# Kernel tuning notes

Measured on AMD Instinct MI355X. Metric: run time of the kernel, lower is better.

The kernel has to match this reference:

```python
import jax, jax.numpy as jnp
import numpy as np

N, E, R, D_IN, D_H, D_OUT = 75000, 1200000, 8, 64, 64, 40


def setup_inputs() -> dict:
    key = jax.random.key(0)
    k_x, k_idx, k_rel, k_w1, k_w2 = jax.random.split(key, 5)
    x = jax.random.normal(k_x, (N, D_IN), dtype=jnp.float32)
    # Regular-degree CSR pointer: ptr[i+1]-ptr[i] = E//N = 16 (nondecreasing, ptr[0]=0, ptr[N]=E)
    ptr = jnp.arange(N + 1, dtype=jnp.int32) * (E // N)
    idx = jax.random.randint(k_idx, (E,), 0, N, dtype=jnp.int32)   # source node per edge
    rel = jax.random.randint(k_rel, (E,), 0, R, dtype=jnp.int32)   # relation type per edge
    W1 = jax.random.normal(k_w1, (R, D_IN, D_H), dtype=jnp.float32) / np.float32(np.sqrt(D_IN))
    W2 = jax.random.normal(k_w2, (R, D_H, D_OUT), dtype=jnp.float32) / np.float32(np.sqrt(D_H))
    return {"x": x, "ptr": ptr, "idx": idx, "rel": rel, "W1": W1, "W2": W2}


def _rgcn_conv(x, W, idx, rel, dst, num_node):
    # Typed transform for every (node, relation) pair: [N, R, F_out]
    xw = jnp.einsum('nd,rdf->nrf', x, W)
    # Per-edge gather of the relation-specific transformed source feature: [E, F_out]
    msg = xw[idx, rel]
    # Scatter-add into destination nodes (CSR rows)
    return jax.ops.segment_sum(msg, dst, num_segments=num_node)


def reference(x, ptr, idx, rel, W1, W2):
    num_edges = idx.shape[0]
    num_node = ptr.shape[0] - 1
    # CSR row id for each edge e: dst[e] = i s.t. ptr[i] <= e < ptr[i+1]
    dst = jnp.searchsorted(ptr, jnp.arange(num_edges, dtype=ptr.dtype), side='right') - 1
    h = _rgcn_conv(x, W1, idx, rel, dst, num_node)
    h = jax.nn.relu(h)  # dropout is identity in eval mode
    h = _rgcn_conv(h, W2, idx, rel, dst, num_node)
    return jax.nn.log_softmax(h, axis=-1)
```

## Files before the change

### kernel.cpp

```cpp
#include <hip/hip_runtime.h>
#include <hip/hip_bf16.h>


typedef __attribute__((ext_vector_type(8))) short short8;
typedef __attribute__((ext_vector_type(4))) float floatx4;

static __device__ __forceinline__ unsigned short f2bf(float f) {
    unsigned u = __float_as_uint(f);
    u += 0x7FFFu + ((u >> 16) & 1u);
    return (unsigned short)(u >> 16);
}
static __device__ __forceinline__ float bf2f(unsigned short h) {
    return __uint_as_float(((unsigned)h) << 16);
}

__global__ void k_cast(const float* __restrict__ x, unsigned short* __restrict__ o,
                       int n4, int np4) {
    int i = blockIdx.x * blockDim.x + threadIdx.x;
    if (i >= np4) return;
    ushort4 r;
    if (i < n4) {
        float4 v = ((const float4*)x)[i];
        r.x = f2bf(v.x); r.y = f2bf(v.y); r.z = f2bf(v.z); r.w = f2bf(v.w);
    } else {
        r.x = r.y = r.z = r.w = 0;
    }
    ((ushort4*)o)[i] = r;
}

__global__ void k_packw(const float* __restrict__ W1, const float* __restrict__ W2,
                        unsigned short* __restrict__ BT1, unsigned short* __restrict__ BT2) {
    int i = blockIdx.x * 256 + threadIdx.x;
    if (i < 512 * 64) {
        int j = i >> 6, d = i & 63;
        int r = j >> 6, f = j & 63;
        BT1[i] = f2bf(W1[r * 4096 + d * 64 + f]);
    } else if (i < 512 * 64 + 320 * 64) {
        int ii = i - 512 * 64;
        int j = ii >> 6, d = ii & 63;
        int r = j / 40, f = j - r * 40;
        BT2[ii] = f2bf(W2[r * 2560 + d * 40 + f]);
    }
}

__global__ __launch_bounds__(256) void k_xw(
    const unsigned short* __restrict__ A, const unsigned short* __restrict__ BT,
    unsigned short* __restrict__ xw, int NC, int nColBlk) {
    int bid = blockIdx.x;
    int cb = bid % nColBlk, rb = bid / nColBlk;
    int wave = threadIdx.x >> 6, lane = threadIdx.x & 63;
    int lr = lane & 15, lg = lane >> 4;
    int rowbase = rb * 256 + wave * 64;
    int col0 = cb * 64;
    floatx4 acc[4][4] = {};
#pragma unroll
    for (int k0 = 0; k0 < 2; ++k0) {
        int koff = k0 * 32 + lg * 8;
        short8 a[4], b[4];
#pragma unroll
        for (int mt = 0; mt < 4; ++mt)
            a[mt] = *(const short8*)(A + (size_t)(rowbase + mt * 16 + lr) * 64 + koff);
#pragma unroll
        for (int nt = 0; nt < 4; ++nt)
            b[nt] = *(const short8*)(BT + (size_t)(col0 + nt * 16 + lr) * 64 + koff);
#pragma unroll
        for (int mt = 0; mt < 4; ++mt)
#pragma unroll
            for (int nt = 0; nt < 4; ++nt)
                acc[mt][nt] = __builtin_amdgcn_mfma_f32_16x16x32_bf16(a[mt], b[nt], acc[mt][nt], 0, 0, 0);
    }
#pragma unroll
    for (int mt = 0; mt < 4; ++mt)
#pragma unroll
        for (int nt = 0; nt < 4; ++nt)
#pragma unroll
            for (int i = 0; i < 4; ++i) {
                int row = rowbase + mt * 16 + lg * 4 + i;
                xw[(size_t)row * NC + col0 + nt * 16 + lr] = f2bf(acc[mt][nt][i]);
            }
}

__global__ __launch_bounds__(256) void k_gs_relu(
    const unsigned short* __restrict__ xw,
    const int* __restrict__ ptr, const int* __restrict__ idx,
    const int* __restrict__ rel,
    unsigned short* __restrict__ H, int M, int MP) {
    int row = blockIdx.x * 4 + (threadIdx.x >> 6);
    int lane = threadIdx.x & 63;
    if (row >= MP) return;
    row = __builtin_amdgcn_readfirstlane(row);
    if (row >= M) { H[(size_t)row * 64 + lane] = 0; return; }
    int ps = ptr[row], pe = ptr[row + 1];
    int deg = pe - ps;
    const int* __restrict__ idxr = idx + ps;
    const int* __restrict__ relr = rel + ps;
    float c = 0.f;
    if (deg == 16) {
        float v[16];
#pragma unroll
        for (int t = 0; t < 16; ++t) {
            size_t o = ((size_t)idxr[t] * 8 + relr[t]) * 64;
            v[t] = bf2f(xw[o + lane]);
        }
#pragma unroll
        for (int t = 0; t < 16; ++t) c += v[t];
    } else {
        for (int t = 0; t < deg; ++t) {
            size_t o = ((size_t)idxr[t] * 8 + relr[t]) * 64;
            c += bf2f(xw[o + lane]);
        }
    }
    H[(size_t)row * 64 + lane] = f2bf(fmaxf(c, 0.f));
}

__global__ __launch_bounds__(256) void k_gs_lsm(
    const unsigned short* __restrict__ xw,
    const int* __restrict__ ptr, const int* __restrict__ idx,
    const int* __restrict__ rel,
    float* __restrict__ out, int M) {
    int row = blockIdx.x * 4 + (threadIdx.x >> 6);
    int lane = threadIdx.x & 63;
    if (row >= M) return;
    row = __builtin_amdgcn_readfirstlane(row);
    int ps = ptr[row], pe = ptr[row + 1];
    int deg = pe - ps;
    const int* __restrict__ idxr = idx + ps;
    const int* __restrict__ relr = rel + ps;
    bool ok = lane < 40;
    int l = ok ? lane : 0;
    float c = 0.f;
    if (deg == 16) {
        float v[16];
#pragma unroll
        for (int t = 0; t < 16; ++t) {
            size_t o = ((size_t)idxr[t] * 8 + relr[t]) * 40;
            v[t] = bf2f(xw[o + l]);
        }
#pragma unroll
        for (int t = 0; t < 16; ++t) c += v[t];
    } else {
        for (int t = 0; t < deg; ++t) {
            size_t o = ((size_t)idxr[t] * 8 + relr[t]) * 40;
            c += bf2f(xw[o + l]);
        }
    }
    float mx = ok ? c : -INFINITY;
#pragma unroll
    for (int m = 1; m < 64; m <<= 1) mx = fmaxf(mx, __shfl_xor(mx, m, 64));
    float e = ok ? __expf(c - mx) : 0.f;
    float s = e;
#pragma unroll
    for (int m = 1; m < 64; m <<= 1) s += __shfl_xor(s, m, 64);
    if (ok) out[(size_t)row * 40 + lane] = c - mx - __logf(s);
}

extern "C" void kernel_launch(void* const* d_in, const int* in_sizes, int n_in,
                              void* d_out, int out_size, void* d_ws, size_t ws_size,
                              hipStream_t stream) {
    const float* x  = (const float*)d_in[0];
    const int* ptr  = (const int*)d_in[1];
    const int* idx  = (const int*)d_in[2];
    const int* rel  = (const int*)d_in[3];
    const float* W1 = (const float*)d_in[4];
    const float* W2 = (const float*)d_in[5];
    float* out = (float*)d_out;

    int N = in_sizes[1] - 1;
    int MP = (N + 255) & ~255;

    char* ws = (char*)d_ws;
    size_t szRow64 = (size_t)MP * 64 * 2;
    unsigned short* xbf  = (unsigned short*)(ws);
    unsigned short* hbf  = (unsigned short*)(ws + szRow64);
    unsigned short* BT1  = (unsigned short*)(ws + 2 * szRow64);
    unsigned short* BT2  = (unsigned short*)(ws + 2 * szRow64 + 512 * 64 * 2);
    unsigned short* xwb  = (unsigned short*)(ws + 2 * szRow64 + 512 * 64 * 2 + 320 * 64 * 2);

    int n4 = N * 16, np4 = MP * 16;
    k_cast<<<(np4 + 255) / 256, 256, 0, stream>>>(x, xbf, n4, np4);
    k_packw<<<(512 * 64 + 320 * 64 + 255) / 256, 256, 0, stream>>>(W1, W2, BT1, BT2);

    int nrb = MP / 256;
    k_xw<<<nrb * 8, 256, 0, stream>>>(xbf, BT1, xwb, 512, 8);
    k_gs_relu<<<MP / 4, 256, 0, stream>>>(xwb, ptr, idx, rel, hbf, N, MP);
    k_xw<<<nrb * 5, 256, 0, stream>>>(hbf, BT2, xwb, 320, 5);
    k_gs_lsm<<<(N + 3) / 4, 256, 0, stream>>>(xwb, ptr, idx, rel, out, N);
}
```

Measured before the change: 129.8 us.

## Fuse fp32-to-bf16 cast into GEMM and gather two rows per wave

Removes the separate cast kernel by loading fp32 x directly in the first transform GEMM and converting to bf16 in registers, with row bounds checks. The two gather-sum kernels now process two destination rows per wavefront, each half-wave loading 4-byte bf16 pairs. This widens each lane's memory access and halves the wave count. The log-softmax reduction moves to 32-lane shuffles over paired features. This trades fewer launches and wider gathers for more index/address logic per wave, and each fp32 row is re-read by every column block of the first GEMM.

```diff
diff --git a/kernel.cpp b/kernel.cpp
--- a/kernel.cpp
+++ b/kernel.cpp
@@ -10,23 +10,8 @@
     u += 0x7FFFu + ((u >> 16) & 1u);
     return (unsigned short)(u >> 16);
 }
-static __device__ __forceinline__ float bf2f(unsigned short h) {
-    return __uint_as_float(((unsigned)h) << 16);
-}
-
-__global__ void k_cast(const float* __restrict__ x, unsigned short* __restrict__ o,
-                       int n4, int np4) {
-    int i = blockIdx.x * blockDim.x + threadIdx.x;
-    if (i >= np4) return;
-    ushort4 r;
-    if (i < n4) {
-        float4 v = ((const float4*)x)[i];
-        r.x = f2bf(v.x); r.y = f2bf(v.y); r.z = f2bf(v.z); r.w = f2bf(v.w);
-    } else {
-        r.x = r.y = r.z = r.w = 0;
-    }
-    ((ushort4*)o)[i] = r;
-}
+static __device__ __forceinline__ float bflo(unsigned u) { return __uint_as_float(u << 16); }
+static __device__ __forceinline__ float bfhi(unsigned u) { return __uint_as_float(u & 0xffff0000u); }
 
 __global__ void k_packw(const float* __restrict__ W1, const float* __restrict__ W2,
                         unsigned short* __restrict__ BT1, unsigned short* __restrict__ BT2) {
@@ -43,9 +28,10 @@
     }
 }
 
+template <int AF32>
 __global__ __launch_bounds__(256) void k_xw(
-    const unsigned short* __restrict__ A, const unsigned short* __restrict__ BT,
-    unsigned short* __restrict__ xw, int NC, int nColBlk) {
+    const void* __restrict__ Av, const unsigned short* __restrict__ BT,
+    unsigned short* __restrict__ xw, int NC, int nColBlk, int M) {
     int bid = blockIdx.x;
     int cb = bid % nColBlk, rb = bid / nColBlk;
     int wave = threadIdx.x >> 6, lane = threadIdx.x & 63;
@@ -58,8 +44,26 @@
         int koff = k0 * 32 + lg * 8;
         short8 a[4], b[4];
 #pragma unroll
-        for (int mt = 0; mt < 4; ++mt)
-            a[mt] = *(const short8*)(A + (size_t)(rowbase + mt * 16 + lr) * 64 + koff);
+        for (int mt = 0; mt < 4; ++mt) {
+            int row = rowbase + mt * 16 + lr;
+            if constexpr (AF32) {
+                const float* Af = (const float*)Av;
+                float4 v0 = {0, 0, 0, 0}, v1 = {0, 0, 0, 0};
+                if (row < M) {
+                    v0 = *(const float4*)(Af + (size_t)row * 64 + koff);
+                    v1 = *(const float4*)(Af + (size_t)row * 64 + koff + 4);
+                }
+                short8 t;
+                t[0] = (short)f2bf(v0.x); t[1] = (short)f2bf(v0.y);
+                t[2] = (short)f2bf(v0.z); t[3] = (short)f2bf(v0.w);
+                t[4] = (short)f2bf(v1.x); t[5] = (short)f2bf(v1.y);
+                t[6] = (short)f2bf(v1.z); t[7] = (short)f2bf(v1.w);
+                a[mt] = t;
+            } else {
+                const unsigned short* Ab = (const unsigned short*)Av;
+                a[mt] = *(const short8*)(Ab + (size_t)row * 64 + koff);
+            }
+        }
 #pragma unroll
         for (int nt = 0; nt < 4; ++nt)
             b[nt] = *(const short8*)(BT + (size_t)(col0 + nt * 16 + lr) * 64 + koff);
@@ -85,32 +89,45 @@
     const int* __restrict__ ptr, const int* __restrict__ idx,
     const int* __restrict__ rel,
     unsigned short* __restrict__ H, int M, int MP) {
-    int row = blockIdx.x * 4 + (threadIdx.x >> 6);
+    int rowA = (blockIdx.x * 4 + (threadIdx.x >> 6)) * 2;
+    if (rowA >= MP) return;
+    rowA = __builtin_amdgcn_readfirstlane(rowA);
     int lane = threadIdx.x & 63;
-    if (row >= MP) return;
-    row = __builtin_amdgcn_readfirstlane(row);
-    if (row >= M) { H[(size_t)row * 64 + lane] = 0; return; }
-    int ps = ptr[row], pe = ptr[row + 1];
-    int deg = pe - ps;
-    const int* __restrict__ idxr = idx + ps;
-    const int* __restrict__ relr = rel + ps;
-    float c = 0.f;
-    if (deg == 16) {
-        float v[16];
+    int fl = lane & 31, eo = lane >> 5;
+    int rowB = rowA + 1;
+    int myrow = eo ? rowB : rowA;
+    if (rowA >= M) {
+        *(unsigned*)(H + (size_t)myrow * 64 + fl * 2) = 0;
+        return;
+    }
+    float cx = 0.f, cy = 0.f;
+    bool both = (rowB < M);
+    int p0 = ptr[rowA], p1 = ptr[rowA + 1];
+    int p2 = both ? ptr[rowA + 2] : p1;
+    if (both && (p1 - p0 == 16) && (p2 - p1 == 16)) {
+        const int* ia = idx + p0; const int* ra_ = rel + p0;
+        const int* ib = idx + p1; const int* rb_ = rel + p1;
+        unsigned u[16];
 #pragma unroll
         for (int t = 0; t < 16; ++t) {
-            size_t o = ((size_t)idxr[t] * 8 + relr[t]) * 64;
-            v[t] = bf2f(xw[o + lane]);
-        }
-#pragma unroll
-        for (int t = 0; t < 16; ++t) c += v[t];
+            size_t bA = ((size_t)ia[t] * 8 + ra_[t]) * 128u;
+            size_t bB = ((size_t)ib[t] * 8 + rb_[t]) * 128u;
+            size_t b = eo ? bB : bA;
+            u[t] = *(const unsigned*)((const char*)xw + b + fl * 4);
+        }
+#pragma unroll
+        for (int t = 0; t < 16; ++t) { cx += bflo(u[t]); cy += bfhi(u[t]); }
     } else {
+        int ps = 0, deg = 0;
+        if (myrow < M) { ps = ptr[myrow]; deg = ptr[myrow + 1] - ps; }
         for (int t = 0; t < deg; ++t) {
-            size_t o = ((size_t)idxr[t] * 8 + relr[t]) * 64;
-            c += bf2f(xw[o + lane]);
-        }
-    }
-    H[(size_t)row * 64 + lane] = f2bf(fmaxf(c, 0.f));
+            int s = idx[ps + t], r = rel[ps + t];
+            unsigned u = *(const unsigned*)((const char*)xw + ((size_t)s * 8 + r) * 128u + fl * 4);
+            cx += bflo(u); cy += bfhi(u);
+        }
+    }
+    unsigned o = ((unsigned)f2bf(fmaxf(cy, 0.f)) << 16) | f2bf(fmaxf(cx, 0.f));
+    *(unsigned*)(H + (size_t)myrow * 64 + fl * 2) = o;
 }
 
 __global__ __launch_bounds__(256) void k_gs_lsm(
@@ -118,40 +135,52 @@
     const int* __restrict__ ptr, const int* __restrict__ idx,
     const int* __restrict__ rel,
     float* __restrict__ out, int M) {
-    int row = blockIdx.x * 4 + (threadIdx.x >> 6);
+    int rowA = (blockIdx.x * 4 + (threadIdx.x >> 6)) * 2;
+    if (rowA >= M) return;
+    rowA = __builtin_amdgcn_readfirstlane(rowA);
     int lane = threadIdx.x & 63;
-    if (row >= M) return;
-    row = __builtin_amdgcn_readfirstlane(row);
-    int ps = ptr[row], pe = ptr[row + 1];
-    int deg = pe - ps;
-    const int* __restrict__ idxr = idx + ps;
-    const int* __restrict__ relr = rel + ps;
-    bool ok = lane < 40;
-    int l = ok ? lane : 0;
-    float c = 0.f;
-    if (deg == 16) {
-        float v[16];
+    int fl = lane & 31, eo = lane >> 5;
+    int rowB = rowA + 1;
+    int myrow = eo ? rowB : rowA;
+    bool okf = fl < 20;
+    int flc = okf ? fl : 0;
+    float cx = 0.f, cy = 0.f;
+    bool both = (rowB < M);
+    int p0 = ptr[rowA], p1 = ptr[rowA + 1];
+    int p2 = both ? ptr[rowA + 2] : p1;
+    if (both && (p1 - p0 == 16) && (p2 - p1 == 16)) {
+        const int* ia = idx + p0; const int* ra_ = rel + p0;
+        const int* ib = idx + p1; const int* rb_ = rel + p1;
+        unsigned u[16];
 #pragma unroll
         for (int t = 0; t < 16; ++t) {
-            size_t o = ((size_t)idxr[t] * 8 + relr[t]) * 40;
-            v[t] = bf2f(xw[o + l]);
-        }
-#pragma unroll
-        for (int t = 0; t < 16; ++t) c += v[t];
+            size_t bA = ((size_t)ia[t] * 8 + ra_[t]) * 80u;
+            size_t bB = ((size_t)ib[t] * 8 + rb_[t]) * 80u;
+            size_t b = eo ? bB : bA;
+            u[t] = *(const unsigned*)((const char*)xw + b + flc * 4);
+        }
+#pragma unroll
+        for (int t = 0; t < 16; ++t) { cx += bflo(u[t]); cy += bfhi(u[t]); }
     } else {
+        int ps = 0, deg = 0;
+        if (myrow < M) { ps = ptr[myrow]; deg = ptr[myrow + 1] - ps; }
         for (int t = 0; t < deg; ++t) {
-            size_t o = ((size_t)idxr[t] * 8 + relr[t]) * 40;
-            c += bf2f(xw[o + l]);
-        }
-    }
-    float mx = ok ? c : -INFINITY;
-#pragma unroll
-    for (int m = 1; m < 64; m <<= 1) mx = fmaxf(mx, __shfl_xor(mx, m, 64));
-    float e = ok ? __expf(c - mx) : 0.f;
-    float s = e;
-#pragma unroll
-    for (int m = 1; m < 64; m <<= 1) s += __shfl_xor(s, m, 64);
-    if (ok) out[(size_t)row * 40 + lane] = c - mx - __logf(s);
+            int s = idx[ps + t], r = rel[ps + t];
+            unsigned u = *(const unsigned*)((const char*)xw + ((size_t)s * 8 + r) * 80u + flc * 4);
+            cx += bflo(u); cy += bfhi(u);
+        }
+    }
+    float mx = okf ? fmaxf(cx, cy) : -INFINITY;
+#pragma unroll
+    for (int m = 1; m < 32; m <<= 1) mx = fmaxf(mx, __shfl_xor(mx, m, 32));
+    float s = okf ? (__expf(cx - mx) + __expf(cy - mx)) : 0.f;
+#pragma unroll
+    for (int m = 1; m < 32; m <<= 1) s += __shfl_xor(s, m, 32);
+    float lse = mx + __logf(s);
+    if (okf && myrow < M) {
+        float2 o = {cx - lse, cy - lse};
+        *(float2*)(out + (size_t)myrow * 40 + flc * 2) = o;
+    }
 }
 
 extern "C" void kernel_launch(void* const* d_in, const int* in_sizes, int n_in,
@@ -170,19 +199,16 @@
 
     char* ws = (char*)d_ws;
     size_t szRow64 = (size_t)MP * 64 * 2;
-    unsigned short* xbf  = (unsigned short*)(ws);
-    unsigned short* hbf  = (unsigned short*)(ws + szRow64);
-    unsigned short* BT1  = (unsigned short*)(ws + 2 * szRow64);
-    unsigned short* BT2  = (unsigned short*)(ws + 2 * szRow64 + 512 * 64 * 2);
-    unsigned short* xwb  = (unsigned short*)(ws + 2 * szRow64 + 512 * 64 * 2 + 320 * 64 * 2);
-
-    int n4 = N * 16, np4 = MP * 16;
-    k_cast<<<(np4 + 255) / 256, 256, 0, stream>>>(x, xbf, n4, np4);
+    unsigned short* hbf = (unsigned short*)ws;
+    unsigned short* BT1 = (unsigned short*)(ws + szRow64);
+    unsigned short* BT2 = BT1 + 512 * 64;
+    unsigned short* xwb = BT2 + 320 * 64;
+
     k_packw<<<(512 * 64 + 320 * 64 + 255) / 256, 256, 0, stream>>>(W1, W2, BT1, BT2);
 
     int nrb = MP / 256;
-    k_xw<<<nrb * 8, 256, 0, stream>>>(xbf, BT1, xwb, 512, 8);
-    k_gs_relu<<<MP / 4, 256, 0, stream>>>(xwb, ptr, idx, rel, hbf, N, MP);
-    k_xw<<<nrb * 5, 256, 0, stream>>>(hbf, BT2, xwb, 320, 5);
-    k_gs_lsm<<<(N + 3) / 4, 256, 0, stream>>>(xwb, ptr, idx, rel, out, N);
-}
+    k_xw<1><<<nrb * 8, 256, 0, stream>>>((const void*)x, BT1, xwb, 512, 8, N);
+    k_gs_relu<<<MP / 8, 256, 0, stream>>>(xwb, ptr, idx, rel, hbf, N, MP);
+    k_xw<0><<<nrb * 5, 256, 0, stream>>>((const void*)hbf, BT2, xwb, 320, 5, MP);
+    k_gs_lsm<<<(N + 7) / 8, 256, 0, stream>>>(xwb, ptr, idx, rel, out, N);
+}
```

Measured after the change: 137.4 us. 5.9% more time.
